# Kernel tuning notes

Hardware: AMD Instinct MI355X
Metric: run time of the kernel (lower is better)

Reference implementation:

```python
import jax, jax.numpy as jnp
import numpy as np
from jax import lax

EPS = 1e-3  # Keras BatchNormalization default epsilon
DN = ('NHWC', 'HWIO', 'NHWC')


def _bn(x, gamma, beta, mean, var):
    inv = gamma * lax.rsqrt(var + EPS)
    return x * inv + (beta - mean * inv)


def setup_inputs() -> dict:
    key = jax.random.key(0)
    ks = jax.random.split(key, 5)
    B, H, W, C = 32, 56, 56, 256
    G, CG = 32, 4  # cardinality, channels per group
    CM = G * CG    # 128 mid channels
    x = jax.random.normal(ks[0], (B, H, W, C), jnp.float32)
    # 32 branch 1x1 convs (256->4 each) stacked -> one 256->128 conv
    w1 = jax.random.normal(ks[1], (1, 1, C, CM), jnp.float32) * 0.05
    b1 = jnp.zeros((CM,), jnp.float32)
    g1 = jnp.ones((CM,), jnp.float32)
    be1 = jnp.zeros((CM,), jnp.float32)
    m1 = jnp.zeros((CM,), jnp.float32)
    v1 = jnp.ones((CM,), jnp.float32)
    # 32 branch 3x3 convs (4->4 each) stacked -> grouped conv kernel [3,3,4,128]
    w2 = jax.random.normal(ks[2], (3, 3, CG, CM), jnp.float32) * 0.1
    b2 = jnp.zeros((CM,), jnp.float32)
    g2 = jnp.ones((CM,), jnp.float32)
    be2 = jnp.zeros((CM,), jnp.float32)
    m2 = jnp.zeros((CM,), jnp.float32)
    v2 = jnp.ones((CM,), jnp.float32)
    # final 1x1 conv 128 -> 256
    w3 = jax.random.normal(ks[3], (1, 1, CM, C), jnp.float32) * 0.05
    b3 = jnp.zeros((C,), jnp.float32)
    return dict(x=x, w1=w1, b1=b1, g1=g1, be1=be1, m1=m1, v1=v1,
                w2=w2, b2=b2, g2=g2, be2=be2, m2=m2, v2=v2,
                w3=w3, b3=b3)


def reference(x, w1, b1, g1, be1, m1, v1, w2, b2, g2, be2, m2, v2, w3, b3):
    # branch 1x1 convs fused: conv 256 -> 128
    h = lax.conv_general_dilated(x, w1, (1, 1), 'SAME', dimension_numbers=DN) + b1
    h = jax.nn.relu(_bn(h, g1, be1, m1, v1))
    # branch 3x3 convs fused: grouped conv, 32 groups of 4 channels
    h = lax.conv_general_dilated(h, w2, (1, 1), 'SAME', dimension_numbers=DN,
                                 feature_group_count=32) + b2
    h = jax.nn.relu(_bn(h, g2, be2, m2, v2))
    # Dropout(0.2) is identity at inference
    # final 1x1 conv 128 -> 256, residual add, relu
    out = lax.conv_general_dilated(h, w3, (1, 1), 'SAME', dimension_numbers=DN) + b3
    return jax.nn.relu(out + x)
```

## Files before the change

kernel.cpp:

```cpp
#include <hip/hip_runtime.h>
#include <stdint.h>

typedef unsigned short u16;
typedef unsigned int   u32;
typedef __attribute__((ext_vector_type(8))) short bf16x8;
typedef __attribute__((ext_vector_type(4))) float f32x4;

#define EPS 1e-3f
#define NB 32
#define HW 56
#define CI 256
#define CM 128
#define PIX (NB*HW*HW)

__device__ __forceinline__ float asf(u32 i){ union{u32 u; float f;} t; t.u=i; return t.f; }
__device__ __forceinline__ u16 f2bf(float f){
  union{float f; u32 u;} t; t.f = f;
  u32 x = t.u;
  return (u16)((x + 0x7fffu + ((x>>16)&1u)) >> 16);
}

__global__ __launch_bounds__(256) void kprep(
    const float* __restrict__ w1, const float* __restrict__ b1, const float* __restrict__ g1,
    const float* __restrict__ be1, const float* __restrict__ m1, const float* __restrict__ v1,
    const float* __restrict__ b2, const float* __restrict__ g2,
    const float* __restrict__ be2, const float* __restrict__ m2, const float* __restrict__ v2,
    const float* __restrict__ w3,
    u16* __restrict__ w1t, u16* __restrict__ w3t,
    float* __restrict__ A1, float* __restrict__ B1,
    float* __restrict__ A2, float* __restrict__ B2){
  int i = blockIdx.x*256 + threadIdx.x;
  if (i < 32768){
    { int n = i >> 8, k = i & 255; w1t[i] = f2bf(w1[k*CM + n]); }
    { int n = i >> 7, k = i & 127; w3t[i] = f2bf(w3[k*CI + n]); }
  }
  if (i < 128){
    float s1 = g1[i] * rsqrtf(v1[i] + EPS);
    A1[i] = s1;
    B1[i] = b1[i]*s1 + be1[i] - m1[i]*s1;
    float s2 = g2[i] * rsqrtf(v2[i] + EPS);
    A2[i] = s2;
    B2[i] = b2[i]*s2 + be2[i] - m2[i]*s2;
  }
}

#define K1_LS 72
__global__ __launch_bounds__(256) void k1(const float* __restrict__ x,
    const u16* __restrict__ w1t, const float* __restrict__ A1v,
    const float* __restrict__ B1v, u16* __restrict__ h1){
  __shared__ __align__(16) char smem[128*K1_LS*2 * 2];
  u16* As = (u16*)smem;
  u16* Bs = (u16*)(smem + 128*K1_LS*2);
  const int tid  = threadIdx.x;
  const int lane = tid & 63, wv = tid >> 6;
  const int col  = lane & 15, quad = lane >> 4;
  const long p0 = (long)blockIdx.x * 128;
  f32x4 acc[8][2];
  #pragma unroll
  for (int a = 0; a < 8; a++)
    #pragma unroll
    for (int b = 0; b < 2; b++){ acc[a][b][0]=0.f; acc[a][b][1]=0.f; acc[a][b][2]=0.f; acc[a][b][3]=0.f; }
  for (int kc = 0; kc < 4; kc++){
    #pragma unroll
    for (int r = 0; r < 8; r++){
      int idx = r*256 + tid;
      int m = idx >> 4, f4 = idx & 15;
      float4 v = *(const float4*)(x + (p0+m)*CI + kc*64 + f4*4);
      u32 lo = (u32)f2bf(v.x) | ((u32)f2bf(v.y) << 16);
      u32 hi = (u32)f2bf(v.z) | ((u32)f2bf(v.w) << 16);
      *(uint2*)(As + m*K1_LS + f4*4) = make_uint2(lo, hi);
    }
    #pragma unroll
    for (int r = 0; r < 4; r++){
      int idx = r*256 + tid;
      int n = idx >> 3, u4 = idx & 7;
      uint4 v = *(const uint4*)(w1t + n*CI + kc*64 + u4*8);
      *(uint4*)(Bs + n*K1_LS + u4*8) = v;
    }
    __syncthreads();
    #pragma unroll
    for (int ks = 0; ks < 2; ks++){
      bf16x8 af[8], bfr[2];
      #pragma unroll
      for (int nt = 0; nt < 2; nt++)
        bfr[nt] = *(const bf16x8*)(Bs + (wv*32 + nt*16 + col)*K1_LS + ks*32 + quad*8);
      #pragma unroll
      for (int mt = 0; mt < 8; mt++)
        af[mt] = *(const bf16x8*)(As + (mt*16 + col)*K1_LS + ks*32 + quad*8);
      #pragma unroll
      for (int mt = 0; mt < 8; mt++)
        #pragma unroll
        for (int nt = 0; nt < 2; nt++)
          acc[mt][nt] = __builtin_amdgcn_mfma_f32_16x16x32_bf16(af[mt], bfr[nt], acc[mt][nt], 0, 0, 0);
    }
    __syncthreads();
  }
  u16* outw = (u16*)smem;
  #pragma unroll
  for (int nt = 0; nt < 2; nt++){
    int n = wv*32 + nt*16 + col;
    float a1 = A1v[n], b1v = B1v[n];
    #pragma unroll
    for (int mt = 0; mt < 8; mt++)
      #pragma unroll
      for (int reg = 0; reg < 4; reg++){
        int m = mt*16 + quad*4 + reg;
        outw[m*136 + n] = f2bf(fmaxf(acc[mt][nt][reg]*a1 + b1v, 0.f));
      }
  }
  __syncthreads();
  #pragma unroll
  for (int r = 0; r < 8; r++){
    int idx = r*256 + tid;
    int m = idx >> 4, u4 = idx & 15;
    uint4 v = *(const uint4*)(outw + m*136 + u4*8);
    *(uint4*)(h1 + (p0+m)*CM + u4*8) = v;
  }
}

#define LSH1 132
#define LSH2 136
__global__ __launch_bounds__(512) void k23(const u16* __restrict__ h1,
    const float* __restrict__ w2, const float* __restrict__ A2v,
    const float* __restrict__ B2v, const u16* __restrict__ w3t,
    const float* __restrict__ b3, const float* __restrict__ x,
    float* __restrict__ out){
  __shared__ __align__(16) char smem[59136 + 112*LSH2*2 + 4608*4];
  u16*  tile = (u16*)smem;
  u16*  h2t  = (u16*)(smem + 59136);
  float* wsh = (float*)(smem + 59136 + 112*LSH2*2);
  float* pre = (float*)smem;

  const int tid = threadIdx.x;
  const int g0 = blockIdx.x * 2;
  const int y0 = g0 % HW;
  const long p0 = (long)g0 * HW;

  for (int i = tid; i < 1152; i += 512)
    ((float4*)wsh)[i] = ((const float4*)w2)[i];
  #pragma unroll
  for (int r = 0; r < 4; r++){
    const int yy = y0 + r - 1;
    const bool valid = (yy >= 0 && yy < HW);
    const uint4* src = (const uint4*)(h1 + (long)(g0 - y0 + yy)*HW*CM);
    for (int i = tid; i < 896; i += 512){
      uint4 v = make_uint4(0u,0u,0u,0u);
      if (valid) v = src[i];
      int px = i >> 4, ch = (i & 15)*8;
      u16* d = tile + (r*HW + px)*LSH1 + ch;
      *(uint2*)d     = make_uint2(v.x, v.y);
      *(uint2*)(d+4) = make_uint2(v.z, v.w);
    }
  }
  __syncthreads();

  {
    const int q   = tid >> 7;
    const int pos = tid & 127;
    if (pos < 112){
      const int r_out = (pos >= HW) ? 1 : 0;
      const int px = pos - r_out*HW;
      int ixo[3]; u32 mk[3];
      #pragma unroll
      for (int kx = 0; kx < 3; kx++){
        int c = px + kx - 1;
        ixo[kx] = (c < 0 ? 0 : (c > 55 ? 55 : c)) * LSH1;
        mk[kx] = (c >= 0 && c < HW) ? 0xffffffffu : 0u;
      }
      float acc[8][4];
      #pragma unroll
      for (int gi = 0; gi < 8; gi++){
        const int cb = (q*8 + gi)*4;
        float a0=0.f, a1=0.f, a2=0.f, a3=0.f;
        #pragma unroll
        for (int ky = 0; ky < 3; ky++){
          const u16* trow = tile + (r_out+ky)*HW*LSH1 + cb;
          #pragma unroll
          for (int kx = 0; kx < 3; kx++){
            uint2 hv = *(const uint2*)(trow + ixo[kx]);
            u32 hx = hv.x & mk[kx], hy = hv.y & mk[kx];
            float i0 = asf(hx<<16), i1 = asf(hx&0xffff0000u);
            float i2 = asf(hy<<16), i3 = asf(hy&0xffff0000u);
            const float* wp = wsh + ((ky*3+kx)*4)*CM + cb;
            float4 w0 = *(const float4*)(wp);
            float4 w1 = *(const float4*)(wp+CM);
            float4 wq2 = *(const float4*)(wp+2*CM);
            float4 wq3 = *(const float4*)(wp+3*CM);
            a0 += i0*w0.x + i1*w1.x + i2*wq2.x + i3*wq3.x;
            a1 += i0*w0.y + i1*w1.y + i2*wq2.y + i3*wq3.y;
            a2 += i0*w0.z + i1*w1.z + i2*wq2.z + i3*wq3.z;
            a3 += i0*w0.w + i1*w1.w + i2*wq2.w + i3*wq3.w;
          }
        }
        acc[gi][0]=a0; acc[gi][1]=a1; acc[gi][2]=a2; acc[gi][3]=a3;
      }
      u16 ov[32];
      #pragma unroll
      for (int gi = 0; gi < 8; gi++)
        #pragma unroll
        for (int co = 0; co < 4; co++){
          int c = q*32 + gi*4 + co;
          ov[gi*4+co] = f2bf(fmaxf(acc[gi][co]*A2v[c] + B2v[c], 0.f));
        }
      u16* op = h2t + pos*LSH2 + q*32;
      #pragma unroll
      for (int v4 = 0; v4 < 4; v4++){
        uint4 pk;
        pk.x = (u32)ov[v4*8+0] | ((u32)ov[v4*8+1]<<16);
        pk.y = (u32)ov[v4*8+2] | ((u32)ov[v4*8+3]<<16);
        pk.z = (u32)ov[v4*8+4] | ((u32)ov[v4*8+5]<<16);
        pk.w = (u32)ov[v4*8+6] | ((u32)ov[v4*8+7]<<16);
        *(uint4*)(op + v4*8) = pk;
      }
    }
  }
  __syncthreads();

  const int lane = tid & 63, wv = tid >> 6;
  const int col  = lane & 15, quad = lane >> 4;
  const int nb = (wv & 3) * 32;
  const int nh = wv >> 2;
  const int ng = nh*128 + nb;
  f32x4 acc3[7][2];
  #pragma unroll
  for (int a = 0; a < 7; a++)
    #pragma unroll
    for (int b = 0; b < 2; b++){ acc3[a][b][0]=0.f; acc3[a][b][1]=0.f; acc3[a][b][2]=0.f; acc3[a][b][3]=0.f; }
  float bias[2] = { b3[ng + col], b3[ng + 16 + col] };
  #pragma unroll
  for (int kc = 0; kc < 4; kc++){
    bf16x8 bfr[2];
    #pragma unroll
    for (int nt = 0; nt < 2; nt++)
      bfr[nt] = *(const bf16x8*)(w3t + (size_t)(ng + nt*16 + col)*CM + kc*32 + quad*8);
    #pragma unroll
    for (int mt = 0; mt < 7; mt++){
      bf16x8 af = *(const bf16x8*)(h2t + (mt*16 + col)*LSH2 + kc*32 + quad*8);
      #pragma unroll
      for (int nt = 0; nt < 2; nt++)
        acc3[mt][nt] = __builtin_amdgcn_mfma_f32_16x16x32_bf16(af, bfr[nt], acc3[mt][nt], 0, 0, 0);
    }
  }
  #pragma unroll
  for (int h = 0; h < 2; h++){
    if (nh == h){
      #pragma unroll
      for (int mt = 0; mt < 7; mt++)
        #pragma unroll
        for (int nt = 0; nt < 2; nt++)
          #pragma unroll
          for (int reg = 0; reg < 4; reg++){
            int m = mt*16 + quad*4 + reg;
            pre[m*132 + nb + nt*16 + col] = acc3[mt][nt][reg] + bias[nt];
          }
    }
    __syncthreads();
    for (int i = tid; i < 3584; i += 512){
      int m = i >> 5, f4 = i & 31;
      float4 pv = *(const float4*)(pre + m*132 + f4*4);
      const float* xr = x + (p0+m)*CI + h*128 + f4*4;
      float4 xv = *(const float4*)xr;
      float4 o;
      o.x = fmaxf(pv.x + xv.x, 0.f);
      o.y = fmaxf(pv.y + xv.y, 0.f);
      o.z = fmaxf(pv.z + xv.z, 0.f);
      o.w = fmaxf(pv.w + xv.w, 0.f);
      *(float4*)(out + (p0+m)*CI + h*128 + f4*4) = o;
    }
    __syncthreads();
  }
}

extern "C" void kernel_launch(void* const* d_in, const int* in_sizes, int n_in,
                              void* d_out, int out_size, void* d_ws, size_t ws_size,
                              hipStream_t stream){
  (void)in_sizes; (void)n_in; (void)out_size; (void)ws_size;
  const float* x   = (const float*)d_in[0];
  const float* w1  = (const float*)d_in[1];
  const float* b1  = (const float*)d_in[2];
  const float* g1  = (const float*)d_in[3];
  const float* be1 = (const float*)d_in[4];
  const float* m1  = (const float*)d_in[5];
  const float* v1  = (const float*)d_in[6];
  const float* w2  = (const float*)d_in[7];
  const float* b2  = (const float*)d_in[8];
  const float* g2  = (const float*)d_in[9];
  const float* be2 = (const float*)d_in[10];
  const float* m2  = (const float*)d_in[11];
  const float* v2  = (const float*)d_in[12];
  const float* w3  = (const float*)d_in[13];
  const float* b3  = (const float*)d_in[14];

  char* ws = (char*)d_ws;
  u16* h1  = (u16*)ws;
  u16* w1t = (u16*)(ws + (size_t)PIX*CM*2);
  u16* w3t = w1t + 32768;
  float* A1 = (float*)(w3t + 32768);
  float* B1 = A1 + 128;
  float* A2 = B1 + 128;
  float* B2 = A2 + 128;

  kprep<<<128, 256, 0, stream>>>(w1,b1,g1,be1,m1,v1,b2,g2,be2,m2,v2,w3,
                                 w1t,w3t,A1,B1,A2,B2);
  k1<<<PIX/128, 256, 0, stream>>>(x, w1t, A1, B1, h1);
  k23<<<NB*HW/2, 512, 0, stream>>>(h1, w2, A2, B2, w3t, b3, x, (float*)d_out);
}
```

Before: 294.5 us.

## Pre-swizzle weights into MFMA fragment order and shrink k23 to one row per block

The prep kernel now writes w1 and w3 in bf16 already arranged in MFMA fragment order, so each lane reads its B operand straight from global memory with one contiguous 16-byte load. This removes the LDS staging of weights in k1. k23 now handles one output row per 256-thread block instead of two rows per 512-thread block. That cuts the halo input rows from 4 to 3 per block, shrinks shared memory, and doubles the grid. The 1x1 output GEMM is retiled to 4x4 MFMA tiles per wave, with zero padding from 56 to 64 rows. The cost is redundant loading of the h1 halo rows (3 rows per output row instead of 2) and MFMA work spent on the padded rows.

```diff
diff --git a/kernel.cpp b/kernel.cpp
--- a/kernel.cpp
+++ b/kernel.cpp
@@ -26,13 +26,23 @@
     const float* __restrict__ b2, const float* __restrict__ g2,
     const float* __restrict__ be2, const float* __restrict__ m2, const float* __restrict__ v2,
     const float* __restrict__ w3,
-    u16* __restrict__ w1t, u16* __restrict__ w3t,
+    u16* __restrict__ w1s, u16* __restrict__ w3s,
     float* __restrict__ A1, float* __restrict__ B1,
     float* __restrict__ A2, float* __restrict__ B2){
   int i = blockIdx.x*256 + threadIdx.x;
   if (i < 32768){
-    { int n = i >> 8, k = i & 255; w1t[i] = f2bf(w1[k*CM + n]); }
-    { int n = i >> 7, k = i & 127; w3t[i] = f2bf(w3[k*CI + n]); }
+    {
+      int j = i & 7, lane = (i >> 3) & 63, kt = (i >> 9) & 7, t = i >> 12;
+      int col = lane & 15, quad = lane >> 4;
+      int n = t*16 + col, k = kt*32 + quad*8 + j;
+      w1s[i] = f2bf(w1[k*CM + n]);
+    }
+    {
+      int j = i & 7, lane = (i >> 3) & 63, kc = (i >> 9) & 3, t = i >> 11;
+      int col = lane & 15, quad = lane >> 4;
+      int n = t*16 + col, k = kc*32 + quad*8 + j;
+      w3s[i] = f2bf(w3[k*CI + n]);
+    }
   }
   if (i < 128){
     float s1 = g1[i] * rsqrtf(v1[i] + EPS);
@@ -46,11 +56,10 @@
 
 #define K1_LS 72
 __global__ __launch_bounds__(256) void k1(const float* __restrict__ x,
-    const u16* __restrict__ w1t, const float* __restrict__ A1v,
+    const u16* __restrict__ w1s, const float* __restrict__ A1v,
     const float* __restrict__ B1v, u16* __restrict__ h1){
-  __shared__ __align__(16) char smem[128*K1_LS*2 * 2];
+  __shared__ __align__(16) char smem[128*136*2];
   u16* As = (u16*)smem;
-  u16* Bs = (u16*)(smem + 128*K1_LS*2);
   const int tid  = threadIdx.x;
   const int lane = tid & 63, wv = tid >> 6;
   const int col  = lane & 15, quad = lane >> 4;
@@ -70,20 +79,14 @@
       u32 hi = (u32)f2bf(v.z) | ((u32)f2bf(v.w) << 16);
       *(uint2*)(As + m*K1_LS + f4*4) = make_uint2(lo, hi);
     }
-    #pragma unroll
-    for (int r = 0; r < 4; r++){
-      int idx = r*256 + tid;
-      int n = idx >> 3, u4 = idx & 7;
-      uint4 v = *(const uint4*)(w1t + n*CI + kc*64 + u4*8);
-      *(uint4*)(Bs + n*K1_LS + u4*8) = v;
-    }
     __syncthreads();
     #pragma unroll
     for (int ks = 0; ks < 2; ks++){
-      bf16x8 af[8], bfr[2];
+      const int kt = kc*2 + ks;
+      bf16x8 bfr[2], af[8];
       #pragma unroll
       for (int nt = 0; nt < 2; nt++)
-        bfr[nt] = *(const bf16x8*)(Bs + (wv*32 + nt*16 + col)*K1_LS + ks*32 + quad*8);
+        bfr[nt] = *(const bf16x8*)(w1s + (size_t)(((wv*2+nt)*8 + kt)*64 + lane)*8);
       #pragma unroll
       for (int mt = 0; mt < 8; mt++)
         af[mt] = *(const bf16x8*)(As + (mt*16 + col)*K1_LS + ks*32 + quad*8);
@@ -120,30 +123,31 @@
 
 #define LSH1 132
 #define LSH2 136
-__global__ __launch_bounds__(512) void k23(const u16* __restrict__ h1,
+__global__ __launch_bounds__(256) void k23(const u16* __restrict__ h1,
     const float* __restrict__ w2, const float* __restrict__ A2v,
-    const float* __restrict__ B2v, const u16* __restrict__ w3t,
+    const float* __restrict__ B2v, const u16* __restrict__ w3s,
     const float* __restrict__ b3, const float* __restrict__ x,
     float* __restrict__ out){
-  __shared__ __align__(16) char smem[59136 + 112*LSH2*2 + 4608*4];
+  __shared__ __align__(16) char smem[3*HW*LSH1*2 + 64*LSH2*2 + 4608*4];
   u16*  tile = (u16*)smem;
-  u16*  h2t  = (u16*)(smem + 59136);
-  float* wsh = (float*)(smem + 59136 + 112*LSH2*2);
+  u16*  h2t  = (u16*)(smem + 3*HW*LSH1*2);
+  float* wsh = (float*)(smem + 3*HW*LSH1*2 + 64*LSH2*2);
   float* pre = (float*)smem;
 
   const int tid = threadIdx.x;
-  const int g0 = blockIdx.x * 2;
-  const int y0 = g0 % HW;
-  const long p0 = (long)g0 * HW;
-
-  for (int i = tid; i < 1152; i += 512)
+  const int y0 = blockIdx.x % HW;
+  const long p0 = (long)blockIdx.x * HW;
+
+  for (int i = tid; i < 1152; i += 256)
     ((float4*)wsh)[i] = ((const float4*)w2)[i];
-  #pragma unroll
-  for (int r = 0; r < 4; r++){
+  for (int i = tid; i < 544; i += 256)
+    ((u32*)(h2t + 56*LSH2))[i] = 0u;
+  #pragma unroll
+  for (int r = 0; r < 3; r++){
     const int yy = y0 + r - 1;
     const bool valid = (yy >= 0 && yy < HW);
-    const uint4* src = (const uint4*)(h1 + (long)(g0 - y0 + yy)*HW*CM);
-    for (int i = tid; i < 896; i += 512){
+    const uint4* src = (const uint4*)(h1 + (long)(blockIdx.x - y0 + yy)*HW*CM);
+    for (int i = tid; i < 896; i += 256){
       uint4 v = make_uint4(0u,0u,0u,0u);
       if (valid) v = src[i];
       int px = i >> 4, ch = (i & 15)*8;
@@ -155,15 +159,13 @@
   __syncthreads();
 
   {
-    const int q   = tid >> 7;
-    const int pos = tid & 127;
-    if (pos < 112){
-      const int r_out = (pos >= HW) ? 1 : 0;
-      const int px = pos - r_out*HW;
+    const int q   = tid >> 6;
+    const int pos = tid & 63;
+    if (pos < HW){
       int ixo[3]; u32 mk[3];
       #pragma unroll
       for (int kx = 0; kx < 3; kx++){
-        int c = px + kx - 1;
+        int c = pos + kx - 1;
         ixo[kx] = (c < 0 ? 0 : (c > 55 ? 55 : c)) * LSH1;
         mk[kx] = (c >= 0 && c < HW) ? 0xffffffffu : 0u;
       }
@@ -174,7 +176,7 @@
         float a0=0.f, a1=0.f, a2=0.f, a3=0.f;
         #pragma unroll
         for (int ky = 0; ky < 3; ky++){
-          const u16* trow = tile + (r_out+ky)*HW*LSH1 + cb;
+          const u16* trow = tile + ky*HW*LSH1 + cb;
           #pragma unroll
           for (int kx = 0; kx < 3; kx++){
             uint2 hv = *(const uint2*)(trow + ixo[kx]);
@@ -218,36 +220,38 @@
 
   const int lane = tid & 63, wv = tid >> 6;
   const int col  = lane & 15, quad = lane >> 4;
-  const int nb = (wv & 3) * 32;
-  const int nh = wv >> 2;
-  const int ng = nh*128 + nb;
-  f32x4 acc3[7][2];
-  #pragma unroll
-  for (int a = 0; a < 7; a++)
-    #pragma unroll
-    for (int b = 0; b < 2; b++){ acc3[a][b][0]=0.f; acc3[a][b][1]=0.f; acc3[a][b][2]=0.f; acc3[a][b][3]=0.f; }
-  float bias[2] = { b3[ng + col], b3[ng + 16 + col] };
+  f32x4 acc3[4][4];
+  #pragma unroll
+  for (int a = 0; a < 4; a++)
+    #pragma unroll
+    for (int b = 0; b < 4; b++){ acc3[a][b][0]=0.f; acc3[a][b][1]=0.f; acc3[a][b][2]=0.f; acc3[a][b][3]=0.f; }
+  float bias[4];
+  #pragma unroll
+  for (int nt = 0; nt < 4; nt++) bias[nt] = b3[wv*64 + nt*16 + col];
   #pragma unroll
   for (int kc = 0; kc < 4; kc++){
-    bf16x8 bfr[2];
-    #pragma unroll
-    for (int nt = 0; nt < 2; nt++)
-      bfr[nt] = *(const bf16x8*)(w3t + (size_t)(ng + nt*16 + col)*CM + kc*32 + quad*8);
-    #pragma unroll
-    for (int mt = 0; mt < 7; mt++){
-      bf16x8 af = *(const bf16x8*)(h2t + (mt*16 + col)*LSH2 + kc*32 + quad*8);
-      #pragma unroll
-      for (int nt = 0; nt < 2; nt++)
-        acc3[mt][nt] = __builtin_amdgcn_mfma_f32_16x16x32_bf16(af, bfr[nt], acc3[mt][nt], 0, 0, 0);
-    }
-  }
+    bf16x8 bfr[4], af[4];
+    #pragma unroll
+    for (int nt = 0; nt < 4; nt++)
+      bfr[nt] = *(const bf16x8*)(w3s + (size_t)(((wv*4+nt)*4 + kc)*64 + lane)*8);
+    #pragma unroll
+    for (int mt = 0; mt < 4; mt++)
+      af[mt] = *(const bf16x8*)(h2t + (mt*16 + col)*LSH2 + kc*32 + quad*8);
+    #pragma unroll
+    for (int mt = 0; mt < 4; mt++)
+      #pragma unroll
+      for (int nt = 0; nt < 4; nt++)
+        acc3[mt][nt] = __builtin_amdgcn_mfma_f32_16x16x32_bf16(af[mt], bfr[nt], acc3[mt][nt], 0, 0, 0);
+  }
+  const int wh = wv >> 1;
+  const int nb = (wv & 1) * 64;
   #pragma unroll
   for (int h = 0; h < 2; h++){
-    if (nh == h){
-      #pragma unroll
-      for (int mt = 0; mt < 7; mt++)
+    if (wh == h){
+      #pragma unroll
+      for (int mt = 0; mt < 4; mt++)
         #pragma unroll
-        for (int nt = 0; nt < 2; nt++)
+        for (int nt = 0; nt < 4; nt++)
           #pragma unroll
           for (int reg = 0; reg < 4; reg++){
             int m = mt*16 + quad*4 + reg;
@@ -255,11 +259,10 @@
           }
     }
     __syncthreads();
-    for (int i = tid; i < 3584; i += 512){
+    for (int i = tid; i < 1792; i += 256){
       int m = i >> 5, f4 = i & 31;
       float4 pv = *(const float4*)(pre + m*132 + f4*4);
-      const float* xr = x + (p0+m)*CI + h*128 + f4*4;
-      float4 xv = *(const float4*)xr;
+      float4 xv = *(const float4*)(x + (p0+m)*CI + h*128 + f4*4);
       float4 o;
       o.x = fmaxf(pv.x + xv.x, 0.f);
       o.y = fmaxf(pv.y + xv.y, 0.f);
@@ -293,15 +296,15 @@
 
   char* ws = (char*)d_ws;
   u16* h1  = (u16*)ws;
-  u16* w1t = (u16*)(ws + (size_t)PIX*CM*2);
-  u16* w3t = w1t + 32768;
-  float* A1 = (float*)(w3t + 32768);
+  u16* w1s = (u16*)(ws + (size_t)PIX*CM*2);
+  u16* w3s = w1s + 32768;
+  float* A1 = (float*)(w3s + 32768);
   float* B1 = A1 + 128;
   float* A2 = B1 + 128;
   float* B2 = A2 + 128;
 
   kprep<<<128, 256, 0, stream>>>(w1,b1,g1,be1,m1,v1,b2,g2,be2,m2,v2,w3,
-                                 w1t,w3t,A1,B1,A2,B2);
-  k1<<<PIX/128, 256, 0, stream>>>(x, w1t, A1, B1, h1);
-  k23<<<NB*HW/2, 512, 0, stream>>>(h1, w2, A2, B2, w3t, b3, x, (float*)d_out);
-}
+                                 w1s,w3s,A1,B1,A2,B2);
+  k1<<<PIX/128, 256, 0, stream>>>(x, w1s, A1, B1, h1);
+  k23<<<NB*HW, 256, 0, stream>>>(h1, w2, A2, B2, w3s, b3, x, (float*)d_out);
+}
```

New measurement: 284.0 us. 1.04x faster.
